# Performance work log

Hardware: AMD Instinct MI355X
Metric: run time of the kernel (lower is better)

The kernel has to match this reference:

```python
import jax, jax.numpy as jnp
import numpy as np

FEATURE_DIM = 256
NUM_STEPS = 3
NUM_GRAPHS = 2048
ATOMS_PER_GRAPH = 64
TOTAL_ATOMS = NUM_GRAPHS * ATOMS_PER_GRAPH


def setup_inputs() -> dict:
    key = jax.random.key(0)
    k_x, k1, k2, k3, k4 = jax.random.split(key, 5)
    H = FEATURE_DIM
    s = 1.0 / np.sqrt(H)
    x = jax.random.normal(k_x, (TOTAL_ATOMS, H), dtype=jnp.float32)
    batch = jnp.repeat(jnp.arange(NUM_GRAPHS, dtype=jnp.int64), ATOMS_PER_GRAPH)
    sizes = jnp.full((NUM_GRAPHS,), ATOMS_PER_GRAPH, dtype=jnp.int64)
    # LSTM params (PyTorch layout: gates ordered i, f, g, o)
    W_ih = jax.random.uniform(k1, (4 * H, H), jnp.float32, -s, s)
    W_hh = jax.random.uniform(k2, (4 * H, H), jnp.float32, -s, s)
    b_ih = jax.random.uniform(k3, (4 * H,), jnp.float32, -s, s)
    b_hh = jax.random.uniform(k4, (4 * H,), jnp.float32, -s, s)
    return {"x": x, "batch": batch, "sizes": sizes,
            "W_ih": W_ih, "W_hh": W_hh, "b_ih": b_ih, "b_hh": b_hh}


def _lstm_cell(u, hx, cx, W_ih, W_hh, b_ih, b_hh):
    # u: input [B,H]; (hx, cx): hidden/cell [B,H]
    gates = u @ W_ih.T + b_ih + hx @ W_hh.T + b_hh  # [B, 4H]
    i, f, g, o = jnp.split(gates, 4, axis=-1)
    i, f, o = jax.nn.sigmoid(i), jax.nn.sigmoid(f), jax.nn.sigmoid(o)
    c = f * cx + i * jnp.tanh(g)
    h = o * jnp.tanh(c)
    return h, c


def _segment_softmax(scores, seg, num_segments):
    m = jax.ops.segment_max(scores, seg, num_segments=num_segments)
    e = jnp.exp(scores - m[seg])
    s = jax.ops.segment_sum(e, seg, num_segments=num_segments)
    return e / s[seg]


def reference(x, batch, sizes, W_ih, W_hh, b_ih, b_hh):
    B = sizes.shape[0]
    H = x.shape[1]
    seg = batch.astype(jnp.int32)
    h = jnp.zeros((B, H), dtype=x.dtype)
    c = jnp.zeros((B, H), dtype=x.dtype)
    q = h
    r = h
    for _ in range(NUM_STEPS):
        # torch code feeds h both as LSTM input and hidden state
        q, c = _lstm_cell(h, h, c, W_ih, W_hh, b_ih, b_hh)
        scores = jnp.sum(x * q[seg], axis=-1)              # [total_atoms]
        attn = _segment_softmax(scores, seg, B)            # per-graph softmax
        r = jax.ops.segment_sum(x * attn[:, None], seg, num_segments=B)  # [B,H]
        h = r  # torch code overwrites the LSTM hidden with r
    return jnp.concatenate([q, r], axis=-1)  # [B, 2H]
```

## Files before the change

kernel.cpp:

```cpp
#include <hip/hip_runtime.h>
#include <math.h>

#define H 256
#define NB 2048
#define APG 64

typedef __attribute__((ext_vector_type(8))) short short8;
typedef __attribute__((ext_vector_type(4))) float f32x4;

__device__ __forceinline__ unsigned short f2bf(float f) {
    unsigned u = __float_as_uint(f);
    u += 0x7fff + ((u >> 16) & 1);
    return (unsigned short)(u >> 16);
}
__device__ __forceinline__ float sigm(float v) { return 1.f / (1.f + __expf(-v)); }

__global__ void prep_kernel(const float* __restrict__ W_ih, const float* __restrict__ W_hh,
                            const float* __restrict__ b_ih, const float* __restrict__ b_hh,
                            unsigned short* __restrict__ Wr, float* __restrict__ br,
                            float* __restrict__ q1, float* __restrict__ c1) {
    int idx = blockIdx.x * 256 + threadIdx.x;
    int wr_row = idx >> 8, k = idx & 255;
    int hcol = wr_row >> 2, gate = wr_row & 3;
    int src = gate * 65536 + hcol * 256 + k;
    Wr[idx] = f2bf(W_ih[src] + W_hh[src]);
    if (blockIdx.x == 0) {
        int t = threadIdx.x;
        float bi  = b_ih[t]       + b_hh[t];
        float bf_ = b_ih[256 + t] + b_hh[256 + t];
        float bg  = b_ih[512 + t] + b_hh[512 + t];
        float bo  = b_ih[768 + t] + b_hh[768 + t];
        br[t * 4 + 0] = bi; br[t * 4 + 1] = bf_;
        br[t * 4 + 2] = bg; br[t * 4 + 3] = bo;
        float cn1 = sigm(bi) * tanhf(bg);
        c1[t] = cn1;
        q1[t] = sigm(bo) * tanhf(cn1);
    }
}

__global__ __launch_bounds__(256)
void gemm_lstm(const unsigned short* __restrict__ hbf, const unsigned short* __restrict__ Wr,
               const float* __restrict__ br, const float* __restrict__ cin, int cins,
               float* __restrict__ cout, float* __restrict__ qdst, int qstride) {
    __shared__ unsigned short smem[2][64 * 128];
    unsigned short* As = smem[0];
    unsigned short* Bs = smem[1];
    int t = threadIdx.x;
    int r0 = blockIdx.y * 64;
    int w0 = blockIdx.x * 64;
    int c0h = blockIdx.x * 16;
    int lane = t & 63, w = t >> 6;
    int ln = lane & 15, qd = lane >> 4;
    int m0 = w * 16;
    f32x4 acc[4] = {};
    for (int kc = 0; kc < 2; ++kc) {
        #pragma unroll
        for (int p = 0; p < 4; ++p) {
            int gid = p * 256 + t;
            int row = gid >> 4, g = gid & 15;
            int sg = g ^ (row & 15);
            *(short8*)&As[row * 128 + sg * 8] =
                *(const short8*)&hbf[(r0 + row) * H + kc * 128 + g * 8];
            *(short8*)&Bs[row * 128 + sg * 8] =
                *(const short8*)&Wr[(w0 + row) * H + kc * 128 + g * 8];
        }
        __syncthreads();
        #pragma unroll
        for (int kk = 0; kk < 4; ++kk) {
            int ga = (kk * 4 + qd) ^ ln;
            short8 a = *(short8*)&As[(m0 + ln) * 128 + ga * 8];
            #pragma unroll
            for (int t4 = 0; t4 < 4; ++t4) {
                short8 b = *(short8*)&Bs[(t4 * 16 + ln) * 128 + ga * 8];
                acc[t4] = __builtin_amdgcn_mfma_f32_16x16x32_bf16(a, b, acc[t4], 0, 0, 0);
            }
        }
        __syncthreads();
    }
    float* gl = (float*)smem;
    #pragma unroll
    for (int t4 = 0; t4 < 4; ++t4)
        #pragma unroll
        for (int r = 0; r < 4; ++r)
            gl[(m0 + qd * 4 + r) * 68 + t4 * 16 + ln] = acc[t4][r];
    __syncthreads();
    #pragma unroll
    for (int p = 0; p < 4; ++p) {
        int idx = p * 256 + t;
        int row = idx >> 4, hc = idx & 15;
        float4 g4 = *(float4*)&gl[row * 68 + hc * 4];
        float4 b4 = *(const float4*)&br[(c0h + hc) * 4];
        float gi = g4.x + b4.x, gf = g4.y + b4.y, gg = g4.z + b4.z, go = g4.w + b4.w;
        float si = sigm(gi), sf = sigm(gf), so = sigm(go);
        float cprev = cin[(r0 + row) * cins + c0h + hc];
        float cn = sf * cprev + si * tanhf(gg);
        if (cout) cout[(r0 + row) * H + c0h + hc] = cn;
        qdst[(r0 + row) * qstride + c0h + hc] = so * tanhf(cn);
    }
}

__global__ __launch_bounds__(256)
void attn(const float* __restrict__ x, const float* __restrict__ qsrc, int qstride,
          unsigned short* __restrict__ hbf_out, float* __restrict__ rout, int rstride) {
    __shared__ float sc[64];
    __shared__ __align__(16) float rpart[4][256];
    int g = blockIdx.x, t = threadIdx.x;
    int lane = t & 63, w = t >> 6;
    const float* xg = x + (size_t)g * APG * H;

    float4 q4 = *(const float4*)&qsrc[(size_t)g * qstride + lane * 4];

    #pragma unroll
    for (int i = 0; i < 16; ++i) {
        int row = i * 4 + w;
        float4 f = *(const float4*)&xg[row * H + lane * 4];
        float p = f.x * q4.x + f.y * q4.y + f.z * q4.z + f.w * q4.w;
        #pragma unroll
        for (int d = 32; d > 0; d >>= 1) p += __shfl_xor(p, d, 64);
        if (lane == 0) sc[row] = p;
    }
    __syncthreads();

    float sv = sc[lane], m = sv;
    #pragma unroll
    for (int d = 32; d > 0; d >>= 1) m = fmaxf(m, __shfl_xor(m, d, 64));
    float e = __expf(sv - m), sum = e;
    #pragma unroll
    for (int d = 32; d > 0; d >>= 1) sum += __shfl_xor(sum, d, 64);
    float pv = e / sum;

    float4 r4 = {0.f, 0.f, 0.f, 0.f};
    #pragma unroll
    for (int i = 0; i < 16; ++i) {
        int row = i * 4 + w;
        float p = __shfl(pv, row, 64);
        float4 f = *(const float4*)&xg[row * H + lane * 4];
        r4.x += p * f.x; r4.y += p * f.y; r4.z += p * f.z; r4.w += p * f.w;
    }
    *(float4*)&rpart[w][lane * 4] = r4;
    __syncthreads();
    float o = rpart[0][t] + rpart[1][t] + rpart[2][t] + rpart[3][t];
    if (hbf_out) hbf_out[(size_t)g * H + t] = f2bf(o);
    if (rout)    rout[(size_t)g * rstride + t] = o;
}

extern "C" void kernel_launch(void* const* d_in, const int* in_sizes, int n_in,
                              void* d_out, int out_size, void* d_ws, size_t ws_size,
                              hipStream_t stream) {
    const float* x    = (const float*)d_in[0];
    const float* W_ih = (const float*)d_in[3];
    const float* W_hh = (const float*)d_in[4];
    const float* b_ih = (const float*)d_in[5];
    const float* b_hh = (const float*)d_in[6];
    float* out = (float*)d_out;

    char* ws = (char*)d_ws;
    unsigned short* Wr   = (unsigned short*)ws;
    float*          br   = (float*)(ws + 524288);
    float*          q1   = (float*)(ws + 528384);
    float*          c1   = (float*)(ws + 529408);
    float*          cbuf = (float*)(ws + 532480);
    float*          qbuf = (float*)(ws + 2629632);
    unsigned short* hbf  = (unsigned short*)(ws + 4726784);

    prep_kernel<<<1024, 256, 0, stream>>>(W_ih, W_hh, b_ih, b_hh, Wr, br, q1, c1);
    attn<<<2048, 256, 0, stream>>>(x, q1, 0, hbf, nullptr, 0);
    gemm_lstm<<<dim3(16, 32), 256, 0, stream>>>(hbf, Wr, br, c1, 0, cbuf, qbuf, 256);
    attn<<<2048, 256, 0, stream>>>(x, qbuf, 256, hbf, nullptr, 0);
    gemm_lstm<<<dim3(16, 32), 256, 0, stream>>>(hbf, Wr, br, cbuf, 256, nullptr, out, 512);
    attn<<<2048, 256, 0, stream>>>(x, out, 512, nullptr, out + 256, 512);
}
```

Before: 302.4 us.

## Fuse weight prep into first attention kernel and keep x tile in registers

Removes the separate prep kernel by having each attention block of the first step compute the initial query from the biases itself and convert a 128-element slice of the combined bf16 weight matrix. All attention kernels now load the 64x256 x tile into registers once and reuse it for both the score dot products and the weighted sum, instead of reading x from memory twice. This saves a kernel launch and half of the x traffic per attention pass, at the cost of 64 extra registers per thread and redundant bias/gate math in every block.

```diff
diff --git a/kernel.cpp b/kernel.cpp
--- a/kernel.cpp
+++ b/kernel.cpp
@@ -14,29 +14,6 @@
     return (unsigned short)(u >> 16);
 }
 __device__ __forceinline__ float sigm(float v) { return 1.f / (1.f + __expf(-v)); }
-
-__global__ void prep_kernel(const float* __restrict__ W_ih, const float* __restrict__ W_hh,
-                            const float* __restrict__ b_ih, const float* __restrict__ b_hh,
-                            unsigned short* __restrict__ Wr, float* __restrict__ br,
-                            float* __restrict__ q1, float* __restrict__ c1) {
-    int idx = blockIdx.x * 256 + threadIdx.x;
-    int wr_row = idx >> 8, k = idx & 255;
-    int hcol = wr_row >> 2, gate = wr_row & 3;
-    int src = gate * 65536 + hcol * 256 + k;
-    Wr[idx] = f2bf(W_ih[src] + W_hh[src]);
-    if (blockIdx.x == 0) {
-        int t = threadIdx.x;
-        float bi  = b_ih[t]       + b_hh[t];
-        float bf_ = b_ih[256 + t] + b_hh[256 + t];
-        float bg  = b_ih[512 + t] + b_hh[512 + t];
-        float bo  = b_ih[768 + t] + b_hh[768 + t];
-        br[t * 4 + 0] = bi; br[t * 4 + 1] = bf_;
-        br[t * 4 + 2] = bg; br[t * 4 + 3] = bo;
-        float cn1 = sigm(bi) * tanhf(bg);
-        c1[t] = cn1;
-        q1[t] = sigm(bo) * tanhf(cn1);
-    }
-}
 
 __global__ __launch_bounds__(256)
 void gemm_lstm(const unsigned short* __restrict__ hbf, const unsigned short* __restrict__ Wr,
@@ -100,24 +77,52 @@
 }
 
 __global__ __launch_bounds__(256)
-void attn(const float* __restrict__ x, const float* __restrict__ qsrc, int qstride,
-          unsigned short* __restrict__ hbf_out, float* __restrict__ rout, int rstride) {
+void attn1(const float* __restrict__ x,
+           const float* __restrict__ W_ih, const float* __restrict__ W_hh,
+           const float* __restrict__ b_ih, const float* __restrict__ b_hh,
+           unsigned short* __restrict__ Wr, float* __restrict__ br,
+           float* __restrict__ c1, unsigned short* __restrict__ hbf_out) {
+    __shared__ float q1s[256];
     __shared__ float sc[64];
     __shared__ __align__(16) float rpart[4][256];
     int g = blockIdx.x, t = threadIdx.x;
     int lane = t & 63, w = t >> 6;
     const float* xg = x + (size_t)g * APG * H;
 
-    float4 q4 = *(const float4*)&qsrc[(size_t)g * qstride + lane * 4];
-
-    #pragma unroll
-    for (int i = 0; i < 16; ++i) {
-        int row = i * 4 + w;
-        float4 f = *(const float4*)&xg[row * H + lane * 4];
-        float p = f.x * q4.x + f.y * q4.y + f.z * q4.z + f.w * q4.w;
+    float4 xa[16];
+    #pragma unroll
+    for (int i = 0; i < 16; ++i)
+        xa[i] = *(const float4*)&xg[(i * 4 + w) * H + lane * 4];
+
+    {
+        float bi  = b_ih[t]       + b_hh[t];
+        float bf_ = b_ih[256 + t] + b_hh[256 + t];
+        float bg  = b_ih[512 + t] + b_hh[512 + t];
+        float bo  = b_ih[768 + t] + b_hh[768 + t];
+        float cn1 = sigm(bi) * tanhf(bg);
+        q1s[t] = sigm(bo) * tanhf(cn1);
+        if (g == 0) {
+            br[t * 4 + 0] = bi; br[t * 4 + 1] = bf_;
+            br[t * 4 + 2] = bg; br[t * 4 + 3] = bo;
+            c1[t] = cn1;
+        }
+        if (t < 128) {
+            int idx = g * 128 + t;
+            int wr_row = idx >> 8, k = idx & 255;
+            int hcol = wr_row >> 2, gate = wr_row & 3;
+            int src = gate * 65536 + hcol * 256 + k;
+            Wr[idx] = f2bf(W_ih[src] + W_hh[src]);
+        }
+    }
+    __syncthreads();
+    float4 q4 = *(float4*)&q1s[lane * 4];
+
+    #pragma unroll
+    for (int i = 0; i < 16; ++i) {
+        float p = xa[i].x * q4.x + xa[i].y * q4.y + xa[i].z * q4.z + xa[i].w * q4.w;
         #pragma unroll
         for (int d = 32; d > 0; d >>= 1) p += __shfl_xor(p, d, 64);
-        if (lane == 0) sc[row] = p;
+        if (lane == 0) sc[i * 4 + w] = p;
     }
     __syncthreads();
 
@@ -132,10 +137,54 @@
     float4 r4 = {0.f, 0.f, 0.f, 0.f};
     #pragma unroll
     for (int i = 0; i < 16; ++i) {
-        int row = i * 4 + w;
-        float p = __shfl(pv, row, 64);
-        float4 f = *(const float4*)&xg[row * H + lane * 4];
-        r4.x += p * f.x; r4.y += p * f.y; r4.z += p * f.z; r4.w += p * f.w;
+        float p = __shfl(pv, i * 4 + w, 64);
+        r4.x += p * xa[i].x; r4.y += p * xa[i].y;
+        r4.z += p * xa[i].z; r4.w += p * xa[i].w;
+    }
+    *(float4*)&rpart[w][lane * 4] = r4;
+    __syncthreads();
+    float o = rpart[0][t] + rpart[1][t] + rpart[2][t] + rpart[3][t];
+    hbf_out[(size_t)g * H + t] = f2bf(o);
+}
+
+__global__ __launch_bounds__(256)
+void attn23(const float* __restrict__ x, const float* __restrict__ qsrc, int qstride,
+            unsigned short* __restrict__ hbf_out, float* __restrict__ rout, int rstride) {
+    __shared__ float sc[64];
+    __shared__ __align__(16) float rpart[4][256];
+    int g = blockIdx.x, t = threadIdx.x;
+    int lane = t & 63, w = t >> 6;
+    const float* xg = x + (size_t)g * APG * H;
+
+    float4 xa[16];
+    #pragma unroll
+    for (int i = 0; i < 16; ++i)
+        xa[i] = *(const float4*)&xg[(i * 4 + w) * H + lane * 4];
+    float4 q4 = *(const float4*)&qsrc[(size_t)g * qstride + lane * 4];
+
+    #pragma unroll
+    for (int i = 0; i < 16; ++i) {
+        float p = xa[i].x * q4.x + xa[i].y * q4.y + xa[i].z * q4.z + xa[i].w * q4.w;
+        #pragma unroll
+        for (int d = 32; d > 0; d >>= 1) p += __shfl_xor(p, d, 64);
+        if (lane == 0) sc[i * 4 + w] = p;
+    }
+    __syncthreads();
+
+    float sv = sc[lane], m = sv;
+    #pragma unroll
+    for (int d = 32; d > 0; d >>= 1) m = fmaxf(m, __shfl_xor(m, d, 64));
+    float e = __expf(sv - m), sum = e;
+    #pragma unroll
+    for (int d = 32; d > 0; d >>= 1) sum += __shfl_xor(sum, d, 64);
+    float pv = e / sum;
+
+    float4 r4 = {0.f, 0.f, 0.f, 0.f};
+    #pragma unroll
+    for (int i = 0; i < 16; ++i) {
+        float p = __shfl(pv, i * 4 + w, 64);
+        r4.x += p * xa[i].x; r4.y += p * xa[i].y;
+        r4.z += p * xa[i].z; r4.w += p * xa[i].w;
     }
     *(float4*)&rpart[w][lane * 4] = r4;
     __syncthreads();
@@ -157,16 +206,14 @@
     char* ws = (char*)d_ws;
     unsigned short* Wr   = (unsigned short*)ws;
     float*          br   = (float*)(ws + 524288);
-    float*          q1   = (float*)(ws + 528384);
-    float*          c1   = (float*)(ws + 529408);
+    float*          c1   = (float*)(ws + 528384);
     float*          cbuf = (float*)(ws + 532480);
     float*          qbuf = (float*)(ws + 2629632);
     unsigned short* hbf  = (unsigned short*)(ws + 4726784);
 
-    prep_kernel<<<1024, 256, 0, stream>>>(W_ih, W_hh, b_ih, b_hh, Wr, br, q1, c1);
-    attn<<<2048, 256, 0, stream>>>(x, q1, 0, hbf, nullptr, 0);
+    attn1<<<2048, 256, 0, stream>>>(x, W_ih, W_hh, b_ih, b_hh, Wr, br, c1, hbf);
     gemm_lstm<<<dim3(16, 32), 256, 0, stream>>>(hbf, Wr, br, c1, 0, cbuf, qbuf, 256);
-    attn<<<2048, 256, 0, stream>>>(x, qbuf, 256, hbf, nullptr, 0);
+    attn23<<<2048, 256, 0, stream>>>(x, qbuf, 256, hbf, nullptr, 0);
     gemm_lstm<<<dim3(16, 32), 256, 0, stream>>>(hbf, Wr, br, cbuf, 256, nullptr, out, 512);
-    attn<<<2048, 256, 0, stream>>>(x, out, 512, nullptr, out + 256, 512);
-}
+    attn23<<<2048, 256, 0, stream>>>(x, out, 512, nullptr, out + 256, 512);
+}
```

Result: faster. 264.3 us (-12.6%).
